# Kernel optimization log

Measured on AMD Instinct MI355X. Metric: run time of the kernel, lower is better.

Reference implementation:

```python
import jax, jax.numpy as jnp
import numpy as np

B, S, D = 4, 2048, 512
H = 8
DH = D // H  # depth per head = 64
SCALE = 1.0 / np.sqrt(np.float32(D))  # NOTE: original divides by sqrt(feature_size), not sqrt(depth)
EPS = 1e-5


def setup_inputs() -> dict:
    key = jax.random.key(0)
    ks = jax.random.split(key, 10)
    std = 1.0 / np.sqrt(D)
    inp = {
        "x": jax.random.normal(ks[0], (B, S, D), dtype=jnp.float32),
        "w_q": jax.random.uniform(ks[1], (D, D), jnp.float32, -std, std),
        "b_q": jax.random.uniform(ks[2], (D,), jnp.float32, -std, std),
        "w_k": jax.random.uniform(ks[3], (D, D), jnp.float32, -std, std),
        "b_k": jax.random.uniform(ks[4], (D,), jnp.float32, -std, std),
        "w_v": jax.random.uniform(ks[5], (D, D), jnp.float32, -std, std),
        "b_v": jax.random.uniform(ks[6], (D,), jnp.float32, -std, std),
        "w_o": jax.random.uniform(ks[7], (D, D), jnp.float32, -std, std),
        "b_o": jax.random.uniform(ks[8], (D,), jnp.float32, -std, std),
        "ln_gamma": jnp.ones((D,), jnp.float32),
        "ln_beta": jnp.zeros((D,), jnp.float32),
    }
    return inp


def _split_heads(t):
    # [B, S, D] -> [B, H, S, DH]
    return t.reshape(B, S, H, DH).transpose(0, 2, 1, 3)


def reference(x, w_q, b_q, w_k, b_k, w_v, b_v, w_o, b_o, ln_gamma, ln_beta):
    q = _split_heads(x @ w_q.T + b_q)
    k = _split_heads(x @ w_k.T + b_k)
    v = _split_heads(x @ w_v.T + b_v)
    # scores: [B, H, S, S], scaled by 1/sqrt(feature_size) per the original
    scores = jnp.einsum("bhqd,bhkd->bhqk", q, k) * SCALE
    alpha = jax.nn.softmax(scores, axis=-1)
    context = jnp.einsum("bhqk,bhkd->bhqd", alpha, v)
    context = context.transpose(0, 2, 1, 3).reshape(B, S, D)
    out = context @ w_o.T + b_o
    # residual + LayerNorm
    y = out + x
    mu = jnp.mean(y, axis=-1, keepdims=True)
    var = jnp.mean(jnp.square(y - mu), axis=-1, keepdims=True)
    y = (y - mu) * jax.lax.rsqrt(var + EPS)
    return y * ln_gamma + ln_beta
```

## Files before the change

kernel.cpp:

```cpp
#include <hip/hip_runtime.h>
#include <hip/hip_bf16.h>
#include <math.h>

#define BB 4
#define SS 2048
#define DD 512
#define HH 8
#define DHH 64
#define MROWS (BB*SS)

constexpr float SCALE  = 0.044194173824159216f;
constexpr float QSCALE = (float)(0.044194173824159216 * 1.4426950408889634);
constexpr float LN_EPS = 1e-5f;

typedef __attribute__((ext_vector_type(8)))  short bf16x8;
typedef __attribute__((ext_vector_type(4)))  float f32x4;
typedef __attribute__((ext_vector_type(16))) float f32x16;

__device__ __forceinline__ ushort f2bf(float f) {
    __hip_bfloat16 h = __float2bfloat16(f);
    ushort u; __builtin_memcpy(&u, &h, 2);
    return u;
}

__device__ __forceinline__ float exp2_hw(float x) {
#if __has_builtin(__builtin_amdgcn_exp2f)
    return __builtin_amdgcn_exp2f(x);
#else
    return exp2f(x);
#endif
}

__device__ __forceinline__ unsigned cvt_pk_bf16(float lo, float hi) {
    unsigned r;
    asm("v_cvt_pk_bf16_f32 %0, %1, %2" : "=v"(r) : "v"(lo), "v"(hi));
    return r;
}
__device__ __forceinline__ void plane_swap(unsigned &a, unsigned &b) {
    asm("v_permlane32_swap_b32 %0, %1" : "+v"(a), "+v"(b));
}
__device__ __forceinline__ bf16x8 pack4(unsigned a0, unsigned a1, unsigned b0, unsigned b1) {
    union { unsigned u[4]; bf16x8 v; } x;
    x.u[0] = a0; x.u[1] = a1; x.u[2] = b0; x.u[3] = b1;
    return x.v;
}

__device__ __forceinline__ void gload16(const void* gsrc, void* lds_dst) {
    __builtin_amdgcn_global_load_lds(
        (const __attribute__((address_space(1))) unsigned int*)gsrc,
        (__attribute__((address_space(3))) unsigned int*)lds_dst,
        16, 0, 0);
}

__global__ __launch_bounds__(256) void cast_kernel(
    const float* __restrict__ x,
    const float* __restrict__ wq, const float* __restrict__ wk,
    const float* __restrict__ wv, const float* __restrict__ wo,
    const float* __restrict__ bq, const float* __restrict__ bk,
    const float* __restrict__ bv,
    ushort* __restrict__ xb, ushort* __restrict__ wb, float* __restrict__ biasc)
{
    const int gid = blockIdx.x * 256 + threadIdx.x;
    if (gid < 1536) {
        float v = gid < 512 ? bq[gid] * QSCALE
                : gid < 1024 ? bk[gid - 512] : bv[gid - 1024];
        biasc[gid] = v;
    }
    const int NX4 = (MROWS * DD) / 4;
    const int NW4 = (DD * DD) / 4;
    const int total = NX4 + 4 * NW4;
    for (int i = gid; i < total; i += gridDim.x * 256) {
        float4 v; ushort4 o;
        if (i < NX4) {
            v = ((const float4*)x)[i];
            o.x = f2bf(v.x); o.y = f2bf(v.y); o.z = f2bf(v.z); o.w = f2bf(v.w);
            ((ushort4*)xb)[i] = o;
        } else {
            int j = i - NX4;
            int which = j >> 16;
            int off = j & 65535;
            const float4* src = which == 0 ? (const float4*)wq
                              : which == 1 ? (const float4*)wk
                              : which == 2 ? (const float4*)wv : (const float4*)wo;
            v = src[off];
            float scl = which == 0 ? QSCALE : 1.0f;
            o.x = f2bf(v.x * scl); o.y = f2bf(v.y * scl);
            o.z = f2bf(v.z * scl); o.w = f2bf(v.w * scl);
            ((ushort4*)wb)[j] = o;
        }
    }
}

__device__ __forceinline__ void stage_tile(const ushort* __restrict__ g, int k0,
                                           ushort* lbuf, int t)
{
    #pragma unroll
    for (int i = 0; i < 4; ++i) {
        int cc = i * 256 + t;
        int row = cc >> 3, slot = cc & 7;
        gload16(g + row * DD + k0 + ((slot ^ (row & 7)) << 3), lbuf + cc * 8);
    }
}

__device__ __forceinline__ void mma_step(const ushort* Abuf, const ushort* Bbuf,
                                         int wr, int wc, int c, int g,
                                         f32x4 (&acc)[4][4])
{
    bf16x8 af[2][4], bf[2][4];
    #pragma unroll
    for (int kc = 0; kc < 2; ++kc) {
        int sw = ((kc * 4 + g) ^ (c & 7)) << 4;
        #pragma unroll
        for (int mi = 0; mi < 4; ++mi)
            af[kc][mi] = *(const bf16x8*)((const char*)Abuf + (wr*64 + mi*16 + c)*128 + sw);
        #pragma unroll
        for (int ni = 0; ni < 4; ++ni)
            bf[kc][ni] = *(const bf16x8*)((const char*)Bbuf + (wc*64 + ni*16 + c)*128 + sw);
    }
    __builtin_amdgcn_s_setprio(1);
    #pragma unroll
    for (int kc = 0; kc < 2; ++kc)
        #pragma unroll
        for (int mi = 0; mi < 4; ++mi)
            #pragma unroll
            for (int ni = 0; ni < 4; ++ni)
                acc[mi][ni] = __builtin_amdgcn_mfma_f32_16x16x32_bf16(
                    af[kc][mi], bf[kc][ni], acc[mi][ni], 0, 0, 0);
    __builtin_amdgcn_s_setprio(0);
}

__global__ __launch_bounds__(256) void qkv_mm(
    const ushort* __restrict__ xb, const ushort* __restrict__ wb,
    const float* __restrict__ biasc,
    ushort* __restrict__ Qb, ushort* __restrict__ Kb, ushort* __restrict__ Vtb)
{
    __shared__ ushort Abuf[128*64];
    __shared__ ushort Bbuf[128*64];
    const int t = threadIdx.x, w = t >> 6, lane = t & 63;
    const int wr = w >> 1, wc = w & 1, c = lane & 15, g = lane >> 4;
    const int nblk = blockIdx.x, mblk = blockIdx.y;

    const ushort* Ag = xb + (size_t)mblk * 128 * DD;
    const ushort* Bg = wb + (size_t)nblk * 128 * DD;

    f32x4 acc[4][4] = {};

    for (int k0 = 0; k0 < DD; k0 += 64) {
        stage_tile(Ag, k0, Abuf, t);
        stage_tile(Bg, k0, Bbuf, t);
        __syncthreads();
        mma_step(Abuf, Bbuf, wr, wc, c, g, acc);
        __syncthreads();
    }

    const int n0 = nblk * 128;
    const int proj = n0 >> 9;
    #pragma unroll
    for (int mi = 0; mi < 4; ++mi) {
        int m = mblk*128 + wr*64 + mi*16 + g*4;
        int bi = m >> 11, s = m & 2047;
        #pragma unroll
        for (int ni = 0; ni < 4; ++ni) {
            int ng = n0 + wc*64 + ni*16 + c;
            float bias = biasc[ng];
            int col = ng & 511, h = col >> 6, d = col & 63;
            if (proj == 2) {
                ushort4 o = { f2bf(acc[mi][ni][0] + bias), f2bf(acc[mi][ni][1] + bias),
                              f2bf(acc[mi][ni][2] + bias), f2bf(acc[mi][ni][3] + bias) };
                *(ushort4*)&Vtb[(((size_t)bi*HH + h)*DHH + d)*SS + s] = o;
            } else {
                ushort* outb = proj == 0 ? Qb : Kb;
                #pragma unroll
                for (int rg = 0; rg < 4; ++rg) {
                    outb[(((size_t)bi*HH + h)*SS + (s + rg))*DHH + d] = f2bf(acc[mi][ni][rg] + bias);
                }
            }
        }
    }
}

__global__ __launch_bounds__(256) void oproj_mm(
    const ushort* __restrict__ ctx, const ushort* __restrict__ wob,
    const float* __restrict__ bo, const float* __restrict__ resid,
    float* __restrict__ out)
{
    __shared__ ushort Abuf[128*64];
    __shared__ ushort Bbuf[128*64];
    const int t = threadIdx.x, w = t >> 6, lane = t & 63;
    const int wr = w >> 1, wc = w & 1, c = lane & 15, g = lane >> 4;
    const int nblk = blockIdx.x, mblk = blockIdx.y;

    const ushort* Ag = ctx + (size_t)mblk * 128 * DD;
    const ushort* Bg = wob + (size_t)nblk * 128 * DD;

    f32x4 acc[4][4] = {};

    for (int k0 = 0; k0 < DD; k0 += 64) {
        stage_tile(Ag, k0, Abuf, t);
        stage_tile(Bg, k0, Bbuf, t);
        __syncthreads();
        mma_step(Abuf, Bbuf, wr, wc, c, g, acc);
        __syncthreads();
    }

    #pragma unroll
    for (int mi = 0; mi < 4; ++mi) {
        int m = mblk*128 + wr*64 + mi*16 + g*4;
        #pragma unroll
        for (int ni = 0; ni < 4; ++ni) {
            int ng = nblk*128 + wc*64 + ni*16 + c;
            float bias = bo[ng];
            #pragma unroll
            for (int rg = 0; rg < 4; ++rg) {
                int mm = m + rg;
                out[(size_t)mm*DD + ng] = acc[mi][ni][rg] + bias + resid[(size_t)mm*DD + ng];
            }
        }
    }
}

__global__ __launch_bounds__(512) void attn_kernel(
    const ushort* __restrict__ Q, const ushort* __restrict__ K,
    const ushort* __restrict__ Vt, ushort* __restrict__ ctx)
{
    __shared__ ushort Ks[2][2][64*64];
    __shared__ ushort Vts[2][2][64*64];

    const int t = threadIdx.x;
    const int w = t >> 6, l = t & 63;
    const int ln31 = l & 31, hi = l >> 5, l7 = l & 7;
    const int qb = w & 3, kvh = w >> 2;

    const int id  = blockIdx.x;
    const int swz = (id & 7) * 64 + (id >> 3);
    const int qt = swz & 15;
    const int h  = (swz >> 4) & 7;
    const int b  = swz >> 7;
    const size_t bh = (size_t)b * HH + h;
    const int q0 = qt*128 + qb*32;

    const ushort* Qp = Q + (bh * SS + (size_t)q0 + ln31) * DHH;
    bf16x8 qf[4];
    #pragma unroll
    for (int s = 0; s < 4; ++s)
        qf[s] = *(const bf16x8*)&Qp[s*16 + hi*8];

    bf16x8 onesf;
    {
        union { short s[8]; bf16x8 v; } u;
        #pragma unroll
        for (int i = 0; i < 8; ++i) u.s[i] = (short)0x3F80;
        onesf = u.v;
    }

    const int t2 = t & 255;
    const int r = t2 >> 3, sl = t2 & 7;
    const int swsl = (sl ^ (r & 7)) << 3;
    const ushort* Kbase  = K  + bh * SS * DHH;
    const ushort* Vtbase = Vt + bh * DHH * SS;
    const int NT = SS/64/2;

#define ATTN_STAGE(kvi, bi_) do {                                          \
        const int tix_ = kvh*NT + (kvi);                                   \
        const ushort* kp_ = Kbase  + (size_t)tix_ * 64 * DHH;              \
        const ushort* vp_ = Vtbase + tix_ * 64;                            \
        _Pragma("unroll")                                                  \
        for (int i_ = 0; i_ < 2; ++i_) {                                   \
            gload16(kp_ + (32*i_ + r)*DHH + swsl,                          \
                    &Ks[kvh][bi_][(32*i_ + r)*64 + sl*8]);                 \
            gload16(vp_ + (size_t)(32*i_ + r)*SS + swsl,                   \
                    &Vts[kvh][bi_][(32*i_ + r)*64 + sl*8]);                \
        }                                                                  \
    } while (0)

    f32x16 ot[2] = {};
    f32x16 zacc  = {};

    ATTN_STAGE(0, 0);

    for (int kv = 0; kv < NT; ++kv) {
        const int cur = kv & 1;
        __syncthreads();
        if (kv + 1 < NT) ATTN_STAGE(kv + 1, cur ^ 1);

        const ushort* Kc = Ks[kvh][cur];
        const ushort* Vc = Vts[kvh][cur];

        f32x16 st[2];
        __builtin_amdgcn_s_setprio(1);
        #pragma unroll
        for (int kt = 0; kt < 2; ++kt) {
            f32x16 z = {};
            #pragma unroll
            for (int s = 0; s < 4; ++s) {
                bf16x8 kf = *(const bf16x8*)((const char*)Kc
                            + (kt*32 + ln31)*128 + (((2*s + hi) ^ l7) << 4));
                z = __builtin_amdgcn_mfma_f32_32x32x16_bf16(kf, qf[s], z, 0, 0, 0);
            }
            st[kt] = z;
        }
        __builtin_amdgcn_s_setprio(0);

        #pragma unroll
        for (int kt = 0; kt < 2; ++kt)
            #pragma unroll
            for (int i = 0; i < 16; ++i)
                st[kt][i] = exp2_hw(st[kt][i]);

        unsigned dk[2][4][2];
        #pragma unroll
        for (int kt = 0; kt < 2; ++kt)
            #pragma unroll
            for (int rb = 0; rb < 4; ++rb) {
                dk[kt][rb][0] = cvt_pk_bf16(st[kt][4*rb+0], st[kt][4*rb+1]);
                dk[kt][rb][1] = cvt_pk_bf16(st[kt][4*rb+2], st[kt][4*rb+3]);
            }
        bf16x8 pb[2][2];
        #pragma unroll
        for (int kt = 0; kt < 2; ++kt)
            #pragma unroll
            for (int s2 = 0; s2 < 2; ++s2) {
                unsigned a0 = dk[kt][2*s2][0], b0 = dk[kt][2*s2+1][0];
                unsigned a1 = dk[kt][2*s2][1], b1 = dk[kt][2*s2+1][1];
                plane_swap(a0, b0);
                plane_swap(a1, b1);
                pb[kt][s2] = pack4(a0, a1, b0, b1);
            }

        __builtin_amdgcn_s_setprio(1);
        #pragma unroll
        for (int kt = 0; kt < 2; ++kt)
            #pragma unroll
            for (int s2 = 0; s2 < 2; ++s2) {
                #pragma unroll
                for (int dt = 0; dt < 2; ++dt) {
                    bf16x8 vf = *(const bf16x8*)((const char*)Vc
                                + (dt*32 + ln31)*128 + (((kt*4 + 2*s2 + hi) ^ l7) << 4));
                    ot[dt] = __builtin_amdgcn_mfma_f32_32x32x16_bf16(vf, pb[kt][s2], ot[dt], 0, 0, 0);
                }
                zacc = __builtin_amdgcn_mfma_f32_32x32x16_bf16(onesf, pb[kt][s2], zacc, 0, 0, 0);
            }
        __builtin_amdgcn_s_setprio(0);
    }
#undef ATTN_STAGE

    __syncthreads();
    float* comb = (float*)&Ks[0][0][0];
    float* p = comb + (size_t)(qb*64 + l) * 33;
    if (kvh == 0) {
        #pragma unroll
        for (int i = 0; i < 16; ++i) { p[i] = ot[0][i]; p[16+i] = ot[1][i]; }
        p[32] = zacc[0];
    }
    __syncthreads();
    if (kvh == 1) {
        const float rl = 1.f / (zacc[0] + p[32]);
        ushort* outp = ctx + ((size_t)b*SS + q0 + ln31) * DD + h*DHH;
        #pragma unroll
        for (int dt = 0; dt < 2; ++dt)
            #pragma unroll
            for (int rb = 0; rb < 4; ++rb) {
                ushort4 o = { f2bf((ot[dt][4*rb+0] + p[dt*16+4*rb+0])*rl),
                              f2bf((ot[dt][4*rb+1] + p[dt*16+4*rb+1])*rl),
                              f2bf((ot[dt][4*rb+2] + p[dt*16+4*rb+2])*rl),
                              f2bf((ot[dt][4*rb+3] + p[dt*16+4*rb+3])*rl) };
                *(ushort4*)&outp[dt*32 + rb*8 + hi*4] = o;
            }
    }
}

__global__ __launch_bounds__(256) void ln_kernel(
    const float* __restrict__ y, const float* __restrict__ gamma,
    const float* __restrict__ beta, float* __restrict__ out)
{
    const int row = blockIdx.x;
    const int t = threadIdx.x;
    const float* yr = y + (size_t)row * DD;

    float2 v = *(const float2*)&yr[t*2];
    float s  = v.x + v.y;
    float sq = v.x*v.x + v.y*v.y;
    #pragma unroll
    for (int off = 1; off < 64; off <<= 1) {
        s  += __shfl_xor(s,  off);
        sq += __shfl_xor(sq, off);
    }
    __shared__ float ss[4], ssq[4];
    int wv = t >> 6;
    if ((t & 63) == 0) { ss[wv] = s; ssq[wv] = sq; }
    __syncthreads();
    s  = ss[0] + ss[1] + ss[2] + ss[3];
    sq = ssq[0] + ssq[1] + ssq[2] + ssq[3];

    float mean = s * (1.0f / DD);
    float var  = sq * (1.0f / DD) - mean * mean;
    float rstd = rsqrtf(var + LN_EPS);

    float2 g  = *(const float2*)&gamma[t*2];
    float2 be = *(const float2*)&beta[t*2];
    float2 o;
    o.x = (v.x - mean) * rstd * g.x + be.x;
    o.y = (v.y - mean) * rstd * g.y + be.y;
    *(float2*)&out[(size_t)row * DD + t*2] = o;
}

extern "C" void kernel_launch(void* const* d_in, const int* in_sizes, int n_in,
                              void* d_out, int out_size, void* d_ws, size_t ws_size,
                              hipStream_t stream)
{
    const float* x     = (const float*)d_in[0];
    const float* wq    = (const float*)d_in[1];
    const float* bq    = (const float*)d_in[2];
    const float* wk    = (const float*)d_in[3];
    const float* bk    = (const float*)d_in[4];
    const float* wv    = (const float*)d_in[5];
    const float* bv    = (const float*)d_in[6];
    const float* wo    = (const float*)d_in[7];
    const float* bo    = (const float*)d_in[8];
    const float* gamma = (const float*)d_in[9];
    const float* beta  = (const float*)d_in[10];

    char* wsb = (char*)d_ws;
    const size_t MB = 1u << 20;
    ushort* xb    = (ushort*)(wsb + 0*MB);
    ushort* wb    = (ushort*)(wsb + 8*MB);
    float*  biasc = (float* )(wsb + 10*MB);
    ushort* Qb    = (ushort*)(wsb + 11*MB);
    ushort* Kb    = (ushort*)(wsb + 19*MB);
    ushort* Vtb   = (ushort*)(wsb + 27*MB);
    ushort* ctxb  = (ushort*)(wsb + 35*MB);
    float*  ybuf  = (float*)(wsb + 11*MB);

    cast_kernel<<<2048, 256, 0, stream>>>(x, wq, wk, wv, wo, bq, bk, bv,
                                          xb, wb, biasc);
    {
        dim3 grid(12, 64);
        qkv_mm<<<grid, 256, 0, stream>>>(xb, wb, biasc, Qb, Kb, Vtb);
    }
    {
        attn_kernel<<<512, 512, 0, stream>>>(Qb, Kb, Vtb, ctxb);
    }
    {
        dim3 grid(4, 64);
        oproj_mm<<<grid, 256, 0, stream>>>(ctxb, wb + 3*DD*DD, bo, x, ybuf);
    }
    ln_kernel<<<MROWS, 256, 0, stream>>>(ybuf, gamma, beta, (float*)d_out);
}
```

Baseline: 105.3 us.

## Pre-tile K and Vt into LDS-ready blocks and compute row sums with VALU

The QKV projection now writes K and V-transposed in a blocked layout of 64-key tiles with 8-element sub-chunks, so the attention kernel can stage each tile with contiguous 16-byte loads and read LDS fragments without an XOR swizzle. The ones-matrix MFMA that accumulated softmax denominators is replaced by a VALU reduction over the exponentiated scores plus a permlane32 swap. The goal is to cut staging address arithmetic and MFMA work in the attention loop. In exchange the denominator is summed in fp32 instead of from bf16-rounded probabilities, which slightly changes numerics, and LDS reads may now hit bank conflicts.

```diff
diff --git a/kernel.cpp b/kernel.cpp
--- a/kernel.cpp
+++ b/kernel.cpp
@@ -37,6 +37,9 @@
     return r;
 }
 __device__ __forceinline__ void plane_swap(unsigned &a, unsigned &b) {
+    asm("v_permlane32_swap_b32 %0, %1" : "+v"(a), "+v"(b));
+}
+__device__ __forceinline__ void plane_swapf(float &a, float &b) {
     asm("v_permlane32_swap_b32 %0, %1" : "+v"(a), "+v"(b));
 }
 __device__ __forceinline__ bf16x8 pack4(unsigned a0, unsigned a1, unsigned b0, unsigned b1) {
@@ -159,21 +162,28 @@
     for (int mi = 0; mi < 4; ++mi) {
         int m = mblk*128 + wr*64 + mi*16 + g*4;
         int bi = m >> 11, s = m & 2047;
+        int tile = s >> 6, row = s & 63, sub = s & 7;
         #pragma unroll
         for (int ni = 0; ni < 4; ++ni) {
             int ng = n0 + wc*64 + ni*16 + c;
             float bias = biasc[ng];
             int col = ng & 511, h = col >> 6, d = col & 63;
             if (proj == 2) {
+                size_t off = ((((size_t)(bi*HH + h)*32 + tile)*8 + (row >> 3))*512)
+                           + d*8 + sub;
                 ushort4 o = { f2bf(acc[mi][ni][0] + bias), f2bf(acc[mi][ni][1] + bias),
                               f2bf(acc[mi][ni][2] + bias), f2bf(acc[mi][ni][3] + bias) };
-                *(ushort4*)&Vtb[(((size_t)bi*HH + h)*DHH + d)*SS + s] = o;
+                *(ushort4*)&Vtb[off] = o;
+            } else if (proj == 1) {
+                size_t base = ((((size_t)(bi*HH + h)*32 + tile)*8 + (d >> 3))*512)
+                            + (d & 7);
+                #pragma unroll
+                for (int rg = 0; rg < 4; ++rg)
+                    Kb[base + (size_t)(row + rg)*8] = f2bf(acc[mi][ni][rg] + bias);
             } else {
-                ushort* outb = proj == 0 ? Qb : Kb;
                 #pragma unroll
-                for (int rg = 0; rg < 4; ++rg) {
-                    outb[(((size_t)bi*HH + h)*SS + (s + rg))*DHH + d] = f2bf(acc[mi][ni][rg] + bias);
-                }
+                for (int rg = 0; rg < 4; ++rg)
+                    Qb[(((size_t)bi*HH + h)*SS + (s + rg))*DHH + d] = f2bf(acc[mi][ni][rg] + bias);
             }
         }
     }
@@ -228,7 +238,7 @@
 
     const int t = threadIdx.x;
     const int w = t >> 6, l = t & 63;
-    const int ln31 = l & 31, hi = l >> 5, l7 = l & 7;
+    const int ln31 = l & 31, hi = l >> 5;
     const int qb = w & 3, kvh = w >> 2;
 
     const int id  = blockIdx.x;
@@ -245,36 +255,21 @@
     for (int s = 0; s < 4; ++s)
         qf[s] = *(const bf16x8*)&Qp[s*16 + hi*8];
 
-    bf16x8 onesf;
-    {
-        union { short s[8]; bf16x8 v; } u;
-        #pragma unroll
-        for (int i = 0; i < 8; ++i) u.s[i] = (short)0x3F80;
-        onesf = u.v;
-    }
-
     const int t2 = t & 255;
-    const int r = t2 >> 3, sl = t2 & 7;
-    const int swsl = (sl ^ (r & 7)) << 3;
-    const ushort* Kbase  = K  + bh * SS * DHH;
-    const ushort* Vtbase = Vt + bh * DHH * SS;
     const int NT = SS/64/2;
 
 #define ATTN_STAGE(kvi, bi_) do {                                          \
-        const int tix_ = kvh*NT + (kvi);                                   \
-        const ushort* kp_ = Kbase  + (size_t)tix_ * 64 * DHH;              \
-        const ushort* vp_ = Vtbase + tix_ * 64;                            \
-        _Pragma("unroll")                                                  \
-        for (int i_ = 0; i_ < 2; ++i_) {                                   \
-            gload16(kp_ + (32*i_ + r)*DHH + swsl,                          \
-                    &Ks[kvh][bi_][(32*i_ + r)*64 + sl*8]);                 \
-            gload16(vp_ + (size_t)(32*i_ + r)*SS + swsl,                   \
-                    &Vts[kvh][bi_][(32*i_ + r)*64 + sl*8]);                \
-        }                                                                  \
+        const size_t tb_ = (bh*32 + (size_t)(kvh*NT + (kvi))) << 12;       \
+        const ushort* kp_ = K  + tb_;                                      \
+        const ushort* vp_ = Vt + tb_;                                      \
+        gload16(kp_ + t2*8,         &Ks[kvh][bi_][t2*8]);                  \
+        gload16(kp_ + (t2+256)*8,   &Ks[kvh][bi_][(t2+256)*8]);            \
+        gload16(vp_ + t2*8,         &Vts[kvh][bi_][t2*8]);                 \
+        gload16(vp_ + (t2+256)*8,   &Vts[kvh][bi_][(t2+256)*8]);           \
     } while (0)
 
     f32x16 ot[2] = {};
-    f32x16 zacc  = {};
+    float lsum = 0.f;
 
     ATTN_STAGE(0, 0);
 
@@ -294,7 +289,7 @@
             #pragma unroll
             for (int s = 0; s < 4; ++s) {
                 bf16x8 kf = *(const bf16x8*)((const char*)Kc
-                            + (kt*32 + ln31)*128 + (((2*s + hi) ^ l7) << 4));
+                            + ((2*s + hi) << 10) + ((kt*32 + ln31) << 4));
                 z = __builtin_amdgcn_mfma_f32_32x32x16_bf16(kf, qf[s], z, 0, 0, 0);
             }
             st[kt] = z;
@@ -306,6 +301,20 @@
             #pragma unroll
             for (int i = 0; i < 16; ++i)
                 st[kt][i] = exp2_hw(st[kt][i]);
+
+        {
+            float ps[16];
+            #pragma unroll
+            for (int i = 0; i < 16; ++i) ps[i] = st[0][i] + st[1][i];
+            #pragma unroll
+            for (int i = 0; i < 8; ++i)  ps[i] += ps[i+8];
+            #pragma unroll
+            for (int i = 0; i < 4; ++i)  ps[i] += ps[i+4];
+            float psum = (ps[0] + ps[1]) + (ps[2] + ps[3]);
+            float pa = psum, pb2 = psum;
+            plane_swapf(pa, pb2);
+            lsum += pa + pb2;
+        }
 
         unsigned dk[2][4][2];
         #pragma unroll
@@ -331,15 +340,13 @@
         #pragma unroll
         for (int kt = 0; kt < 2; ++kt)
             #pragma unroll
-            for (int s2 = 0; s2 < 2; ++s2) {
+            for (int s2 = 0; s2 < 2; ++s2)
                 #pragma unroll
                 for (int dt = 0; dt < 2; ++dt) {
                     bf16x8 vf = *(const bf16x8*)((const char*)Vc
-                                + (dt*32 + ln31)*128 + (((kt*4 + 2*s2 + hi) ^ l7) << 4));
+                                + ((kt*4 + 2*s2 + hi) << 10) + ((dt*32 + ln31) << 4));
                     ot[dt] = __builtin_amdgcn_mfma_f32_32x32x16_bf16(vf, pb[kt][s2], ot[dt], 0, 0, 0);
                 }
-                zacc = __builtin_amdgcn_mfma_f32_32x32x16_bf16(onesf, pb[kt][s2], zacc, 0, 0, 0);
-            }
         __builtin_amdgcn_s_setprio(0);
     }
 #undef ATTN_STAGE
@@ -350,11 +357,11 @@
     if (kvh == 0) {
         #pragma unroll
         for (int i = 0; i < 16; ++i) { p[i] = ot[0][i]; p[16+i] = ot[1][i]; }
-        p[32] = zacc[0];
+        p[32] = lsum;
     }
     __syncthreads();
     if (kvh == 1) {
-        const float rl = 1.f / (zacc[0] + p[32]);
+        const float rl = 1.f / (lsum + p[32]);
         ushort* outp = ctx + ((size_t)b*SS + q0 + ln31) * DD + h*DHH;
         #pragma unroll
         for (int dt = 0; dt < 2; ++dt)
```

Result: no change. 104.1 us (-1.1%).
